# Performance work log

Hardware: AMD Instinct MI355X
Metric: run time of the kernel (lower is better)

## Reference

```python
import jax, jax.numpy as jnp
import numpy as np


def setup_inputs() -> dict:
    key = jax.random.key(0)
    k1, k2, k3, k4 = jax.random.split(key, 4)
    B = 1048576        # batch of annotator ids
    A = 65536          # num_annotators
    D = 8              # latent_dims
    annotator = jax.random.randint(k1, (B,), 0, A, dtype=jnp.int64)
    posterior_mu = jax.random.normal(k2, (A, D), dtype=jnp.float32)
    posterior_covtril = jax.random.normal(k3, (A, D, D), dtype=jnp.float32)
    eps = jax.random.normal(k4, (B, D), dtype=jnp.float32)
    return {
        "annotator": annotator,
        "posterior_mu": posterior_mu,
        "posterior_covtril": posterior_covtril,
        "eps": eps,
    }


def reference(annotator, posterior_mu, posterior_covtril, eps):
    # Batched equivalent of the per-annotator MVN rsample loop:
    #   z_i = mu[a_i] + tril(covtril[a_i]) @ eps_i
    mu = posterior_mu[annotator]                 # [B, D]   gather
    L = jnp.tril(posterior_covtril[annotator])   # [B, D, D] gather + tril mask
    z = mu + jnp.einsum("bij,bj->bi", L, eps)    # reparameterized sample
    return z
```

## Files before the change

### kernel.cpp

```cpp
#include <hip/hip_runtime.h>
#include <hip/hip_bf16.h>
#include <hip/hip_fp16.h>


#define A_CNT 65536

typedef float    f32x4 __attribute__((ext_vector_type(4)));
typedef _Float16 f16x8 __attribute__((ext_vector_type(8)));


__global__ __launch_bounds__(256) void pack_kernel(
    const float* __restrict__ mu,
    const float* __restrict__ L,
    _Float16* __restrict__ rec,
    int A)
{
    int a = blockIdx.x * blockDim.x + threadIdx.x;
    if (a >= A) return;

    const f32x4* muv = reinterpret_cast<const f32x4*>(mu + (size_t)a * 8);
    const f32x4* Lv  = reinterpret_cast<const f32x4*>(L + (size_t)a * 64);
    f32x4 m0 = __builtin_nontemporal_load(muv);
    f32x4 m1 = __builtin_nontemporal_load(muv + 1);
    f32x4 r0 = __builtin_nontemporal_load(Lv + 0);
    f32x4 r1 = __builtin_nontemporal_load(Lv + 2);
    f32x4 r2 = __builtin_nontemporal_load(Lv + 4);
    f32x4 r3 = __builtin_nontemporal_load(Lv + 6);
    f32x4 r4a = __builtin_nontemporal_load(Lv + 8),  r4b = __builtin_nontemporal_load(Lv + 9);
    f32x4 r5a = __builtin_nontemporal_load(Lv + 10), r5b = __builtin_nontemporal_load(Lv + 11);
    f32x4 r6a = __builtin_nontemporal_load(Lv + 12), r6b = __builtin_nontemporal_load(Lv + 13);
    f32x4 r7a = __builtin_nontemporal_load(Lv + 14), r7b = __builtin_nontemporal_load(Lv + 15);

    f16x8 ch[8];
    #pragma unroll
    for (int j = 0; j < 4; ++j) {
        ch[0][j] = (_Float16)m0[j];  ch[0][4+j] = (_Float16)m1[j];
        ch[1][j] = (_Float16)r0[j];  ch[1][4+j] = (_Float16)r1[j];
        ch[2][j] = (_Float16)r2[j];  ch[2][4+j] = (_Float16)r3[j];
        ch[3][j] = (_Float16)r4a[j]; ch[3][4+j] = (_Float16)r4b[j];
        ch[4][j] = (_Float16)r5a[j]; ch[4][4+j] = (_Float16)r5b[j];
        ch[5][j] = (_Float16)r6a[j]; ch[5][4+j] = (_Float16)r6b[j];
        ch[6][j] = (_Float16)r7a[j]; ch[6][4+j] = (_Float16)r7b[j];
        ch[7][j] = (_Float16)0.f;    ch[7][4+j] = (_Float16)0.f;
    }
    f16x8* o = reinterpret_cast<f16x8*>(rec + (size_t)a * 64);
    #pragma unroll
    for (int c = 0; c < 8; ++c) __builtin_nontemporal_store(ch[c], o + c);
}

__global__ __launch_bounds__(256) void lv_kernel_coop(
    const int* __restrict__ ann,
    const _Float16* __restrict__ rec,
    const float* __restrict__ eps,
    float* __restrict__ out,
    int B)
{
    __shared__ __align__(16) char lds_raw[4 * 64 * 128];

    const int lane = threadIdx.x & 63;
    const int wave = threadIdx.x >> 6;
    const int b_base = (blockIdx.x * 4 + wave) * 64;
    char* lw = lds_raw + wave * (64 * 128);

    const int c = lane & 7;
    const int rhi = lane >> 3;
    #pragma unroll
    for (int k = 0; k < 8; ++k) {
        const int r = 8 * k + rhi;
        const int brow = b_base + r;
        int a = 0;
        if (brow < B) a = ann[brow];
        const f16x8 chunk = *reinterpret_cast<const f16x8*>(
            rec + (size_t)a * 64 + c * 8);
        *reinterpret_cast<f16x8*>(lw + r * 128 + ((c ^ (r & 7)) << 4)) = chunk;
    }
    __syncthreads();

    const int b = b_base + lane;
    if (b >= B) return;

    const f32x4* epsv = reinterpret_cast<const f32x4*>(eps + (size_t)b * 8);
    const f32x4 e0 = __builtin_nontemporal_load(epsv);
    const f32x4 e1 = __builtin_nontemporal_load(epsv + 1);
    const float e[8] = {e0[0], e0[1], e0[2], e0[3], e1[0], e1[1], e1[2], e1[3]};

    f16x8 ch[7];
    #pragma unroll
    for (int cc = 0; cc < 7; ++cc) {
        ch[cc] = *reinterpret_cast<const f16x8*>(
            lw + lane * 128 + ((cc ^ (lane & 7)) << 4));
    }

    float z[8];
    #pragma unroll
    for (int i = 0; i < 8; ++i) z[i] = (float)ch[0][i];
    #pragma unroll
    for (int i = 0; i < 4; ++i) {
        #pragma unroll
        for (int j = 0; j <= i; ++j)
            z[i] += (float)ch[1 + (i >> 1)][(i & 1) * 4 + j] * e[j];
    }
    #pragma unroll
    for (int i = 4; i < 8; ++i) {
        #pragma unroll
        for (int j = 0; j <= i; ++j)
            z[i] += (float)ch[3 + (i - 4)][j] * e[j];
    }

    f32x4* outv = reinterpret_cast<f32x4*>(out + (size_t)b * 8);
    f32x4 o0 = {z[0], z[1], z[2], z[3]};
    f32x4 o1 = {z[4], z[5], z[6], z[7]};
    __builtin_nontemporal_store(o0, outv);
    __builtin_nontemporal_store(o1, outv + 1);
}

__global__ __launch_bounds__(256) void lv_kernel_f32(
    const int* __restrict__ ann,
    const float* __restrict__ mu,
    const float* __restrict__ L,
    const float* __restrict__ eps,
    float* __restrict__ out,
    int B)
{
    int b = blockIdx.x * blockDim.x + threadIdx.x;
    if (b >= B) return;
    const int a = ann[b];
    const f32x4* epsv = reinterpret_cast<const f32x4*>(eps + (size_t)b * 8);
    const f32x4 e0 = epsv[0];
    const f32x4 e1 = epsv[1];
    const float e[8] = {e0[0], e0[1], e0[2], e0[3], e1[0], e1[1], e1[2], e1[3]};
    const f32x4* muv = reinterpret_cast<const f32x4*>(mu + (size_t)a * 8);
    const f32x4 m0 = muv[0];
    const f32x4 m1 = muv[1];
    float z[8] = {m0[0], m0[1], m0[2], m0[3], m1[0], m1[1], m1[2], m1[3]};
    const f32x4* Lv = reinterpret_cast<const f32x4*>(L + (size_t)a * 64);
    #pragma unroll
    for (int i = 0; i < 4; ++i) {
        const f32x4 r0 = Lv[i * 2];
        #pragma unroll
        for (int j = 0; j <= i; ++j) z[i] += r0[j] * e[j];
    }
    #pragma unroll
    for (int i = 4; i < 8; ++i) {
        const f32x4 r0 = Lv[i * 2];
        const f32x4 r1 = Lv[i * 2 + 1];
        const float r[8] = {r0[0], r0[1], r0[2], r0[3], r1[0], r1[1], r1[2], r1[3]};
        #pragma unroll
        for (int j = 0; j <= i; ++j) z[i] += r[j] * e[j];
    }
    f32x4* outv = reinterpret_cast<f32x4*>(out + (size_t)b * 8);
    f32x4 o0 = {z[0], z[1], z[2], z[3]};
    f32x4 o1 = {z[4], z[5], z[6], z[7]};
    outv[0] = o0;
    outv[1] = o1;
}

extern "C" void kernel_launch(void* const* d_in, const int* in_sizes, int n_in,
                              void* d_out, int out_size, void* d_ws, size_t ws_size,
                              hipStream_t stream) {
    const int*   ann = (const int*)d_in[0];
    const float* mu  = (const float*)d_in[1];
    const float* L   = (const float*)d_in[2];
    const float* eps = (const float*)d_in[3];
    float* out = (float*)d_out;

    const int B = in_sizes[0];
    const int A = in_sizes[1] / 8;

    const size_t rec_bytes = (size_t)A * 64 * sizeof(_Float16);
    if (ws_size >= rec_bytes) {
        _Float16* rec = (_Float16*)d_ws;
        pack_kernel<<<(A + 255) / 256, 256, 0, stream>>>(mu, L, rec, A);
        const int blocks = (B + 255) / 256;
        lv_kernel_coop<<<blocks, 256, 0, stream>>>(ann, rec, eps, out, B);
    } else {
        const int blocks = (B + 255) / 256;
        lv_kernel_f32<<<blocks, 256, 0, stream>>>(ann, mu, L, eps, out, B);
    }
}
```

Measured before the change: 54.41 us.

## Gather packed records straight into LDS with global_load_lds, two rows per lane

Replaces the cooperative gather-then-transpose kernel with one that uses global_load_lds to DMA each 16-byte chunk of a packed fp16 record directly into LDS in a chunk-major layout. Each 64-thread block handles 128 rows, two per lane, and waits with a single vmcnt wait instead of a barrier. This drops the VGPR round trip and the XOR-swizzle writes, and overlaps the two rows' gathers. In exchange each lane now issues small strided 16B scattered loads rather than 8-lane coalesced 128B row reads, which may use the memory system less efficiently, and the tiny blocks may affect occupancy.

```diff
diff --git a/kernel.cpp b/kernel.cpp
--- a/kernel.cpp
+++ b/kernel.cpp
@@ -7,7 +7,6 @@
 
 typedef float    f32x4 __attribute__((ext_vector_type(4)));
 typedef _Float16 f16x8 __attribute__((ext_vector_type(8)));
-
 
 __global__ __launch_bounds__(256) void pack_kernel(
     const float* __restrict__ mu,
@@ -48,70 +47,99 @@
     for (int c = 0; c < 8; ++c) __builtin_nontemporal_store(ch[c], o + c);
 }
 
-__global__ __launch_bounds__(256) void lv_kernel_coop(
+__device__ __forceinline__ void compute_row(const f16x8 ch[7], const float e[8],
+                                            float z[8]) {
+    #pragma unroll
+    for (int i = 0; i < 8; ++i) z[i] = (float)ch[0][i];
+    #pragma unroll
+    for (int i = 0; i < 4; ++i) {
+        #pragma unroll
+        for (int j = 0; j <= i; ++j)
+            z[i] += (float)ch[1 + (i >> 1)][(i & 1) * 4 + j] * e[j];
+    }
+    #pragma unroll
+    for (int i = 4; i < 8; ++i) {
+        #pragma unroll
+        for (int j = 0; j <= i; ++j)
+            z[i] += (float)ch[3 + (i - 4)][j] * e[j];
+    }
+}
+
+__global__ __launch_bounds__(64) void lv_lds(
     const int* __restrict__ ann,
     const _Float16* __restrict__ rec,
     const float* __restrict__ eps,
     float* __restrict__ out,
     int B)
 {
-    __shared__ __align__(16) char lds_raw[4 * 64 * 128];
-
-    const int lane = threadIdx.x & 63;
-    const int wave = threadIdx.x >> 6;
-    const int b_base = (blockIdx.x * 4 + wave) * 64;
-    char* lw = lds_raw + wave * (64 * 128);
-
-    const int c = lane & 7;
-    const int rhi = lane >> 3;
-    #pragma unroll
-    for (int k = 0; k < 8; ++k) {
-        const int r = 8 * k + rhi;
-        const int brow = b_base + r;
-        int a = 0;
-        if (brow < B) a = ann[brow];
-        const f16x8 chunk = *reinterpret_cast<const f16x8*>(
-            rec + (size_t)a * 64 + c * 8);
-        *reinterpret_cast<f16x8*>(lw + r * 128 + ((c ^ (r & 7)) << 4)) = chunk;
-    }
-    __syncthreads();
-
-    const int b = b_base + lane;
-    if (b >= B) return;
-
-    const f32x4* epsv = reinterpret_cast<const f32x4*>(eps + (size_t)b * 8);
-    const f32x4 e0 = __builtin_nontemporal_load(epsv);
-    const f32x4 e1 = __builtin_nontemporal_load(epsv + 1);
-    const float e[8] = {e0[0], e0[1], e0[2], e0[3], e1[0], e1[1], e1[2], e1[3]};
-
-    f16x8 ch[7];
-    #pragma unroll
-    for (int cc = 0; cc < 7; ++cc) {
-        ch[cc] = *reinterpret_cast<const f16x8*>(
-            lw + lane * 128 + ((cc ^ (lane & 7)) << 4));
-    }
-
-    float z[8];
-    #pragma unroll
-    for (int i = 0; i < 8; ++i) z[i] = (float)ch[0][i];
-    #pragma unroll
-    for (int i = 0; i < 4; ++i) {
-        #pragma unroll
-        for (int j = 0; j <= i; ++j)
-            z[i] += (float)ch[1 + (i >> 1)][(i & 1) * 4 + j] * e[j];
-    }
-    #pragma unroll
-    for (int i = 4; i < 8; ++i) {
-        #pragma unroll
-        for (int j = 0; j <= i; ++j)
-            z[i] += (float)ch[3 + (i - 4)][j] * e[j];
-    }
-
-    f32x4* outv = reinterpret_cast<f32x4*>(out + (size_t)b * 8);
-    f32x4 o0 = {z[0], z[1], z[2], z[3]};
-    f32x4 o1 = {z[4], z[5], z[6], z[7]};
-    __builtin_nontemporal_store(o0, outv);
-    __builtin_nontemporal_store(o1, outv + 1);
+    __shared__ __align__(16) char lds[2 * 7 * 1024];
+
+    const int lane = threadIdx.x;
+    const long base = (long)blockIdx.x * 128;
+    const long b0 = base + lane;
+    const long b1 = base + 64 + lane;
+
+    int a0 = 0, a1 = 0;
+    if (b0 < (long)B) a0 = __builtin_nontemporal_load(ann + b0);
+    if (b1 < (long)B) a1 = __builtin_nontemporal_load(ann + b1);
+
+    const char* r0 = (const char*)rec + (size_t)a0 * 128;
+    const char* r1 = (const char*)rec + (size_t)a1 * 128;
+
+    #pragma unroll
+    for (int c = 0; c < 7; ++c)
+        __builtin_amdgcn_global_load_lds(
+            (const __attribute__((address_space(1))) void*)(r0 + c * 16),
+            (__attribute__((address_space(3))) void*)(lds + c * 1024),
+            16, 0, 0);
+    #pragma unroll
+    for (int c = 0; c < 7; ++c)
+        __builtin_amdgcn_global_load_lds(
+            (const __attribute__((address_space(1))) void*)(r1 + c * 16),
+            (__attribute__((address_space(3))) void*)(lds + 7168 + c * 1024),
+            16, 0, 0);
+
+    const long bc0 = (b0 < (long)B) ? b0 : 0;
+    const long bc1 = (b1 < (long)B) ? b1 : 0;
+    const f32x4* e0p = reinterpret_cast<const f32x4*>(eps + (size_t)bc0 * 8);
+    const f32x4* e1p = reinterpret_cast<const f32x4*>(eps + (size_t)bc1 * 8);
+    const f32x4 e00 = __builtin_nontemporal_load(e0p);
+    const f32x4 e01 = __builtin_nontemporal_load(e0p + 1);
+    const f32x4 e10 = __builtin_nontemporal_load(e1p);
+    const f32x4 e11 = __builtin_nontemporal_load(e1p + 1);
+
+    asm volatile("s_waitcnt vmcnt(0)" ::: "memory");
+
+    if (b0 < (long)B) {
+        f16x8 ch[7];
+        #pragma unroll
+        for (int c = 0; c < 7; ++c)
+            ch[c] = *reinterpret_cast<const f16x8*>(lds + c * 1024 + lane * 16);
+        const float e[8] = {e00[0], e00[1], e00[2], e00[3],
+                            e01[0], e01[1], e01[2], e01[3]};
+        float z[8];
+        compute_row(ch, e, z);
+        f32x4* outv = reinterpret_cast<f32x4*>(out + (size_t)b0 * 8);
+        f32x4 o0 = {z[0], z[1], z[2], z[3]};
+        f32x4 o1 = {z[4], z[5], z[6], z[7]};
+        __builtin_nontemporal_store(o0, outv);
+        __builtin_nontemporal_store(o1, outv + 1);
+    }
+    if (b1 < (long)B) {
+        f16x8 ch[7];
+        #pragma unroll
+        for (int c = 0; c < 7; ++c)
+            ch[c] = *reinterpret_cast<const f16x8*>(lds + 7168 + c * 1024 + lane * 16);
+        const float e[8] = {e10[0], e10[1], e10[2], e10[3],
+                            e11[0], e11[1], e11[2], e11[3]};
+        float z[8];
+        compute_row(ch, e, z);
+        f32x4* outv = reinterpret_cast<f32x4*>(out + (size_t)b1 * 8);
+        f32x4 o0 = {z[0], z[1], z[2], z[3]};
+        f32x4 o1 = {z[4], z[5], z[6], z[7]};
+        __builtin_nontemporal_store(o0, outv);
+        __builtin_nontemporal_store(o1, outv + 1);
+    }
 }
 
 __global__ __launch_bounds__(256) void lv_kernel_f32(
@@ -171,8 +199,8 @@
     if (ws_size >= rec_bytes) {
         _Float16* rec = (_Float16*)d_ws;
         pack_kernel<<<(A + 255) / 256, 256, 0, stream>>>(mu, L, rec, A);
-        const int blocks = (B + 255) / 256;
-        lv_kernel_coop<<<blocks, 256, 0, stream>>>(ann, rec, eps, out, B);
+        const int blocks = (B + 127) / 128;
+        lv_lds<<<blocks, 64, 0, stream>>>(ann, rec, eps, out, B);
     } else {
         const int blocks = (B + 255) / 256;
         lv_kernel_f32<<<blocks, 256, 0, stream>>>(ann, mu, L, eps, out, B);
```

Result: slower. 58.11 us (+6.8%).
